# Performance work log

Measured on AMD Instinct MI355X. Metric: run time of the kernel, lower is better.

## Reference

```python
import jax, jax.numpy as jnp
import numpy as np

C = 256
EPS = 1e-5


def dwconv3x3(x, w):
    # x: [B,C,H,W], w: [C,1,3,3] depthwise (groups=C)
    return jax.lax.conv_general_dilated(
        x, w, window_strides=(1, 1), padding=((1, 1), (1, 1)),
        dimension_numbers=('NCHW', 'OIHW', 'NCHW'), feature_group_count=x.shape[1])


def bn(x, gamma, beta, mean, var):
    # inference-mode batchnorm over channel dim of NCHW
    inv = gamma * jax.lax.rsqrt(var + EPS)
    return x * inv[:, None, None] + (beta - mean * inv)[:, None, None]


def setup_inputs() -> dict:
    key = jax.random.key(0)
    ks = jax.random.split(key, 8)
    B, H, W = 32, 64, 64
    inp = {
        'x': jax.random.normal(ks[0], (B, C, H, W), jnp.float32),
        'edge_w': jax.random.normal(ks[1], (C, 1, 3, 3), jnp.float32) * 0.1,
        'edge_gamma': jnp.ones((C,), jnp.float32),
        'edge_beta': jnp.zeros((C,), jnp.float32),
        'edge_mean': jnp.zeros((C,), jnp.float32),
        'edge_var': jnp.ones((C,), jnp.float32),
        'fc1_w': jax.random.normal(ks[2], (C // 16, C), jnp.float32) * 0.05,
        'fc2_w': jax.random.normal(ks[3], (C, C // 16), jnp.float32) * 0.05,
        'fusion_w': jax.random.normal(ks[4], (C, 2 * C), jnp.float32) * 0.05,
        'fusion_b': jnp.zeros((C,), jnp.float32),
        'bn1_gamma': jnp.ones((C,), jnp.float32),
        'bn1_beta': jnp.zeros((C,), jnp.float32),
        'bn1_mean': jnp.zeros((C,), jnp.float32),
        'bn1_var': jnp.ones((C,), jnp.float32),
        'deform_w': jax.random.normal(ks[5], (C, 1, 3, 3), jnp.float32) * 0.1,
        'balance_w': jax.random.normal(ks[6], (C, C), jnp.float32) * 0.05,
        'balance_b': jnp.zeros((C,), jnp.float32),
        'bn2_gamma': jnp.ones((C,), jnp.float32),
        'bn2_beta': jnp.zeros((C,), jnp.float32),
        'bn2_mean': jnp.zeros((C,), jnp.float32),
        'bn2_var': jnp.ones((C,), jnp.float32),
    }
    return inp


def reference(x, edge_w, edge_gamma, edge_beta, edge_mean, edge_var,
              fc1_w, fc2_w, fusion_w, fusion_b,
              bn1_gamma, bn1_beta, bn1_mean, bn1_var,
              deform_w, balance_w, balance_b,
              bn2_gamma, bn2_beta, bn2_mean, bn2_var):
    # --- EdgeEnhancementAttention ---
    edge = jax.nn.relu(bn(dwconv3x3(x, edge_w), edge_gamma, edge_beta, edge_mean, edge_var))
    # SE channel attention
    avg = jnp.mean(x, axis=(2, 3))                       # [B,C]
    att = jax.nn.relu(avg @ fc1_w.T)                     # [B,C/16]
    att = jax.nn.sigmoid(att @ fc2_w.T)                  # [B,C]
    enhanced = x * att[:, :, None, None]
    fused = jnp.concatenate([enhanced, edge], axis=1)    # [B,2C,H,W]
    out = jnp.einsum('bchw,oc->bohw', fused, fusion_w) + fusion_b[None, :, None, None]
    out = bn(out, bn1_gamma, bn1_beta, bn1_mean, bn1_var)
    # --- DeformConv2d with zero offsets == plain depthwise 3x3 conv, no bias ---
    out = dwconv3x3(out, deform_w)
    # --- balance: 1x1 conv + BN, then gate by input ---
    out = jnp.einsum('bchw,oc->bohw', out, balance_w) + balance_b[None, :, None, None]
    out = bn(out, bn2_gamma, bn2_beta, bn2_mean, bn2_var)
    return out * x
```

## Files before the change

kernel.cpp:

```cpp
#include <hip/hip_runtime.h>
#include <math.h>

#define HW 4096
#define PLSTRIDE ((size_t)HW * 8)

typedef unsigned short ushort_t;
typedef short v8s __attribute__((ext_vector_type(8)));
typedef float v4f __attribute__((ext_vector_type(4)));

__device__ __forceinline__ float bf2f(ushort_t u) {
    union { unsigned int i; float f; } v; v.i = ((unsigned int)u) << 16; return v.f;
}
__device__ __forceinline__ ushort_t f2bf(float f) {
    unsigned int x = __float_as_uint(f);
    x += 0x7fffu + ((x >> 16) & 1u);
    return (ushort_t)(x >> 16);
}

__device__ __forceinline__ void gld16(const ushort_t* g, ushort_t* l) {
    __builtin_amdgcn_global_load_lds(
        (__attribute__((address_space(1))) void*)g,
        (__attribute__((address_space(3))) void*)l, 16, 0, 0);
}

__global__ __launch_bounds__(256) void k_consts(
    const float* eg, const float* ebt, const float* em, const float* ev,
    const float* fb,
    const float* g1, const float* b1, const float* m1, const float* v1,
    const float* balb,
    const float* g2, const float* b2, const float* m2, const float* v2,
    float* cbuf)
{
    int c = threadIdx.x;
    float iE = eg[c] * rsqrtf(ev[c] + 1e-5f);
    cbuf[c]       = iE;
    cbuf[256 + c] = ebt[c] - em[c] * iE;
    float i1 = g1[c] * rsqrtf(v1[c] + 1e-5f);
    cbuf[512 + c] = i1;
    cbuf[768 + c] = b1[c] - m1[c] * i1 + fb[c] * i1;
    float i2 = g2[c] * rsqrtf(v2[c] + 1e-5f);
    cbuf[1024 + c] = i2;
    cbuf[1280 + c] = b2[c] - m2[c] * i2 + balb[c] * i2;
}

__global__ __launch_bounds__(256) void k_wcopy(const float* fusw, const float* balw,
                                               ushort_t* fusw2b, ushort_t* balwb)
{
    int o = blockIdx.x, t = threadIdx.x;
    fusw2b[o * 256 + t] = f2bf(fusw[o * 512 + 256 + t]);
    balwb[o * 256 + t]  = f2bf(balw[o * 256 + t]);
}

__global__ __launch_bounds__(512) void k_edge(const float* x, const float* ew,
                                              const float* cbuf, ushort_t* A,
                                              float* avg)
{
    __shared__ __align__(16) ushort_t Xs[4096];
    __shared__ __align__(16) ushort_t Es[4096];
    int cg = blockIdx.x;
    int b = blockIdx.y;
    int t = threadIdx.x;
    int w = t & 63;
    int pl = t >> 6;
    int c = cg * 8 + pl;
    const float* px = x + ((size_t)(b * 256 + c)) * HW;
    ushort_t* AX = A + ((size_t)(b * 64 + cg)) * PLSTRIDE;
    ushort_t* AE = A + ((size_t)(b * 64 + 32 + cg)) * PLSTRIDE;
    float wt[9];
    #pragma unroll
    for (int k = 0; k < 9; ++k) wt[k] = ew[c * 9 + k];
    float sE = cbuf[c], cE = cbuf[256 + c];
    bool wl = (w > 0), wrr = (w < 63);

    float p0l = 0.f, p0c = 0.f, p0r = 0.f;
    float p1l, p1c, p1r;
    p1c = px[w];
    p1l = wl ? px[w - 1] : 0.f;
    p1r = wrr ? px[w + 1] : 0.f;
    float s = 0.f;
    for (int hb = 0; hb < 8; ++hb) {
        #pragma unroll
        for (int hi = 0; hi < 8; ++hi) {
            int h = hb * 8 + hi;
            float p2l, p2c, p2r;
            if (h < 63) {
                const float* row = px + (h + 1) * 64;
                p2c = row[w];
                p2l = wl ? row[w - 1] : 0.f;
                p2r = wrr ? row[w + 1] : 0.f;
            } else {
                p2l = p2c = p2r = 0.f;
            }
            float a = p0l * wt[0] + p0c * wt[1] + p0r * wt[2]
                    + p1l * wt[3] + p1c * wt[4] + p1r * wt[5]
                    + p2l * wt[6] + p2c * wt[7] + p2r * wt[8];
            s += p1c;
            float v = a * sE + cE;
            Es[hi * 512 + w * 8 + pl] = f2bf(v > 0.f ? v : 0.f);
            Xs[hi * 512 + w * 8 + pl] = f2bf(p1c);
            p0l = p1l; p0c = p1c; p0r = p1r;
            p1l = p2l; p1c = p2c; p1r = p2r;
        }
        __syncthreads();
        {
            int hwg = (hb * 8 + pl) * 64 + w;
            uint4 vx = *(const uint4*)&Xs[pl * 512 + w * 8];
            uint4 ve = *(const uint4*)&Es[pl * 512 + w * 8];
            *(uint4*)(AX + (size_t)hwg * 8) = vx;
            *(uint4*)(AE + (size_t)hwg * 8) = ve;
        }
        __syncthreads();
    }
    #pragma unroll
    for (int off = 32; off > 0; off >>= 1) s += __shfl_down(s, off, 64);
    if ((t & 63) == 0) avg[b * 256 + c] = s * (1.0f / HW);
}

__global__ __launch_bounds__(256) void k_sefold(const float* avg, const float* fc1,
                                                const float* fc2, const float* fusw,
                                                ushort_t* w1b)
{
    int b = blockIdx.x, t = threadIdx.x;
    __shared__ float av[256];
    __shared__ float hid[16];
    av[t] = avg[b * 256 + t];
    __syncthreads();
    if (t < 16) {
        float h = 0.f;
        for (int c = 0; c < 256; ++c) h += av[c] * fc1[t * 256 + c];
        hid[t] = h > 0.f ? h : 0.f;
    }
    __syncthreads();
    float a = 0.f;
    #pragma unroll
    for (int j = 0; j < 16; ++j) a += hid[j] * fc2[t * 16 + j];
    float att = 1.0f / (1.0f + expf(-a));
    ushort_t* wout = w1b + (size_t)b * 65536;
    for (int o = 0; o < 256; ++o)
        wout[o * 256 + t] = f2bf(fusw[o * 512 + t] * att);
}

__global__ __launch_bounds__(512) void k_gemm1(ushort_t* A, const ushort_t* w1b,
                                               const ushort_t* fusw2b,
                                               const float* cbuf)
{
    __shared__ __align__(16) ushort_t At[2][128 * 64];
    int hw0 = blockIdx.x * 128;
    int b = blockIdx.y;
    int t = threadIdx.x;
    int lane = t & 63, wv = t >> 6;
    int quad = lane >> 4, l16 = lane & 15;
    int wr = wv >> 2, wc = wv & 3;

    v4f acc[4][4];
    #pragma unroll
    for (int i = 0; i < 4; ++i)
        #pragma unroll
        for (int j = 0; j < 4; ++j) acc[i][j] = (v4f){0.f, 0.f, 0.f, 0.f};

    const ushort_t* rowA[4];
    const ushort_t* rowB[4];
    int oo[4];
    #pragma unroll
    for (int nt = 0; nt < 4; ++nt) {
        int o = wc * 64 + nt * 16 + l16;
        oo[nt] = o;
        rowA[nt] = w1b + ((size_t)(b * 256 + o)) * 256;
        rowB[nt] = fusw2b + (size_t)o * 256;
    }

    int mrow0 = wv * 16 + (lane >> 3);
    int cswz = (lane & 7) ^ (mrow0 & 7);
    const ushort_t* srcK = A + ((size_t)(b * 64 + cswz)) * PLSTRIDE
                             + ((size_t)(hw0 + mrow0)) * 8;

#define STAGE1(bs, kbv) { \
    const ushort_t* sp = srcK + (size_t)((kbv) * 8) * PLSTRIDE; \
    gld16(sp, &At[bs][(wv * 16) * 64]); \
    gld16(sp + 64, &At[bs][(wv * 16 + 8) * 64]); }

#define LDB1(dst, kbv) { \
    _Pragma("unroll") for (int ks2 = 0; ks2 < 2; ++ks2) { \
        int kg = (kbv) * 64 + ks2 * 32 + quad * 8; \
        _Pragma("unroll") for (int nt = 0; nt < 4; ++nt) { \
            dst[ks2][nt] = ((kbv) < 4) ? *(const v8s*)(rowA[nt] + kg) \
                                       : *(const v8s*)(rowB[nt] + (kg - 256)); \
        } } }

#define COMP1(bs, bsrc) { \
    _Pragma("unroll") for (int ks2 = 0; ks2 < 2; ++ks2) { \
        v8s afr[4]; \
        _Pragma("unroll") for (int mt = 0; mt < 4; ++mt) { \
            int ml = wr * 64 + mt * 16 + l16; \
            int jj = (ks2 * 4 + quad) ^ (ml & 7); \
            afr[mt] = *(const v8s*)(&At[bs][ml * 64 + jj * 8]); \
        } \
        _Pragma("unroll") for (int mt = 0; mt < 4; ++mt) \
            _Pragma("unroll") for (int nt = 0; nt < 4; ++nt) \
                acc[mt][nt] = __builtin_amdgcn_mfma_f32_16x16x32_bf16( \
                    afr[mt], bsrc[ks2][nt], acc[mt][nt], 0, 0, 0); \
    } }

    v8s bq0[2][4], bq1[2][4];
    LDB1(bq0, 0);
    STAGE1(0, 0);
    __syncthreads();
    #pragma unroll
    for (int kb = 0; kb < 8; ++kb) {
        if ((kb & 1) == 0) {
            if (kb < 7) { STAGE1(1, kb + 1); LDB1(bq1, kb + 1); }
            COMP1(0, bq0);
        } else {
            if (kb < 7) { STAGE1(0, kb + 1); LDB1(bq0, kb + 1); }
            COMP1(1, bq1);
        }
        __syncthreads();
    }
#undef STAGE1
#undef LDB1
#undef COMP1

    #pragma unroll
    for (int nt = 0; nt < 4; ++nt) {
        int o = oo[nt];
        float s1 = cbuf[512 + o], c1 = cbuf[768 + o];
        ushort_t* op = A + ((size_t)(b * 64 + 32 + (o >> 3))) * PLSTRIDE + (o & 7);
        #pragma unroll
        for (int mt = 0; mt < 4; ++mt)
            #pragma unroll
            for (int r = 0; r < 4; ++r) {
                int m = hw0 + wr * 64 + mt * 16 + quad * 4 + r;
                op[(size_t)m * 8] = f2bf(acc[mt][nt][r] * s1 + c1);
            }
    }
}

__global__ __launch_bounds__(256) void k_dw2(ushort_t* A, const float* dfw)
{
    int h = blockIdx.x;
    int b = blockIdx.y;
    int t = threadIdx.x;
    int wc = t & 7;
    int cg = t >> 3;
    int c0 = cg * 8;
    int w0 = wc * 8;

    float acc[8][8];
    #pragma unroll
    for (int w = 0; w < 8; ++w)
        #pragma unroll
        for (int ch = 0; ch < 8; ++ch) acc[w][ch] = 0.f;

    const ushort_t* pE = A + ((size_t)(b * 64 + 32 + cg)) * PLSTRIDE;
    #pragma unroll
    for (int r = 0; r < 3; ++r) {
        int hh = h - 1 + r;
        if (hh < 0 || hh > 63) continue;
        float wtr[3][8];
        #pragma unroll
        for (int d = 0; d < 3; ++d)
            #pragma unroll
            for (int ch = 0; ch < 8; ++ch)
                wtr[d][ch] = dfw[(c0 + ch) * 9 + r * 3 + d];
        const ushort_t* row = pE + (size_t)(hh * 64) * 8;
        uint4 rv[10];
        #pragma unroll
        for (int j = 0; j < 10; ++j) {
            int col = w0 - 1 + j;
            if (col >= 0 && col < 64)
                rv[j] = *(const uint4*)(row + (size_t)col * 8);
            else
                rv[j] = (uint4){0u, 0u, 0u, 0u};
        }
        #pragma unroll
        for (int j = 0; j < 10; ++j) {
            unsigned int wd[4] = { rv[j].x, rv[j].y, rv[j].z, rv[j].w };
            float v[8];
            #pragma unroll
            for (int i = 0; i < 8; ++i)
                v[i] = bf2f((i & 1) ? (ushort_t)(wd[i >> 1] >> 16)
                                    : (ushort_t)(wd[i >> 1] & 0xffff));
            if (j <= 7)
                #pragma unroll
                for (int ch = 0; ch < 8; ++ch) acc[j][ch] += v[ch] * wtr[0][ch];
            if (j >= 1 && j <= 8)
                #pragma unroll
                for (int ch = 0; ch < 8; ++ch) acc[j - 1][ch] += v[ch] * wtr[1][ch];
            if (j >= 2)
                #pragma unroll
                for (int ch = 0; ch < 8; ++ch) acc[j - 2][ch] += v[ch] * wtr[2][ch];
        }
    }
    ushort_t* pX = A + ((size_t)(b * 64 + cg)) * PLSTRIDE + (size_t)(h * 64 + w0) * 8;
    #pragma unroll
    for (int w = 0; w < 8; ++w) {
        uint4 ov;
        ov.x = (unsigned int)f2bf(acc[w][0]) | ((unsigned int)f2bf(acc[w][1]) << 16);
        ov.y = (unsigned int)f2bf(acc[w][2]) | ((unsigned int)f2bf(acc[w][3]) << 16);
        ov.z = (unsigned int)f2bf(acc[w][4]) | ((unsigned int)f2bf(acc[w][5]) << 16);
        ov.w = (unsigned int)f2bf(acc[w][6]) | ((unsigned int)f2bf(acc[w][7]) << 16);
        *(uint4*)(pX + (size_t)w * 8) = ov;
    }
}

__global__ __launch_bounds__(512) void k_gemm2(ushort_t* A, const ushort_t* balwb)
{
    __shared__ __align__(16) ushort_t At[2][128 * 64];
    int hw0 = blockIdx.x * 128;
    int b = blockIdx.y;
    int t = threadIdx.x;
    int lane = t & 63, wv = t >> 6;
    int quad = lane >> 4, l16 = lane & 15;
    int wr = wv >> 2, wc = wv & 3;

    v4f acc[4][4];
    #pragma unroll
    for (int i = 0; i < 4; ++i)
        #pragma unroll
        for (int j = 0; j < 4; ++j) acc[i][j] = (v4f){0.f, 0.f, 0.f, 0.f};

    const ushort_t* rowW[4];
    int oo[4];
    #pragma unroll
    for (int nt = 0; nt < 4; ++nt) {
        int o = wc * 64 + nt * 16 + l16;
        oo[nt] = o;
        rowW[nt] = balwb + (size_t)o * 256;
    }

    int mrow0 = wv * 16 + (lane >> 3);
    int cswz = (lane & 7) ^ (mrow0 & 7);
    const ushort_t* srcK = A + ((size_t)(b * 64 + cswz)) * PLSTRIDE
                             + ((size_t)(hw0 + mrow0)) * 8;

#define STAGE2(bs, kbv) { \
    const ushort_t* sp = srcK + (size_t)((kbv) * 8) * PLSTRIDE; \
    gld16(sp, &At[bs][(wv * 16) * 64]); \
    gld16(sp + 64, &At[bs][(wv * 16 + 8) * 64]); }

#define LDB2(dst, kbv) { \
    _Pragma("unroll") for (int ks2 = 0; ks2 < 2; ++ks2) { \
        int kg = (kbv) * 64 + ks2 * 32 + quad * 8; \
        _Pragma("unroll") for (int nt = 0; nt < 4; ++nt) \
            dst[ks2][nt] = *(const v8s*)(rowW[nt] + kg); \
    } }

#define COMP2(bs, bsrc) { \
    _Pragma("unroll") for (int ks2 = 0; ks2 < 2; ++ks2) { \
        v8s afr[4]; \
        _Pragma("unroll") for (int mt = 0; mt < 4; ++mt) { \
            int ml = wr * 64 + mt * 16 + l16; \
            int jj = (ks2 * 4 + quad) ^ (ml & 7); \
            afr[mt] = *(const v8s*)(&At[bs][ml * 64 + jj * 8]); \
        } \
        _Pragma("unroll") for (int mt = 0; mt < 4; ++mt) \
            _Pragma("unroll") for (int nt = 0; nt < 4; ++nt) \
                acc[mt][nt] = __builtin_amdgcn_mfma_f32_16x16x32_bf16( \
                    afr[mt], bsrc[ks2][nt], acc[mt][nt], 0, 0, 0); \
    } }

    v8s bq0[2][4], bq1[2][4];
    LDB2(bq0, 0);
    STAGE2(0, 0);
    __syncthreads();
    #pragma unroll
    for (int kb = 0; kb < 4; ++kb) {
        if ((kb & 1) == 0) {
            if (kb < 3) { STAGE2(1, kb + 1); LDB2(bq1, kb + 1); }
            COMP2(0, bq0);
        } else {
            if (kb < 3) { STAGE2(0, kb + 1); LDB2(bq0, kb + 1); }
            COMP2(1, bq1);
        }
        __syncthreads();
    }
#undef STAGE2
#undef LDB2
#undef COMP2

    #pragma unroll
    for (int nt = 0; nt < 4; ++nt) {
        int o = oo[nt];
        ushort_t* op = A + ((size_t)(b * 64 + 32 + (o >> 3))) * PLSTRIDE + (o & 7);
        #pragma unroll
        for (int mt = 0; mt < 4; ++mt)
            #pragma unroll
            for (int r = 0; r < 4; ++r) {
                int m = hw0 + wr * 64 + mt * 16 + quad * 4 + r;
                op[(size_t)m * 8] = f2bf(acc[mt][nt][r]);
            }
    }
}

__global__ __launch_bounds__(256) void k_final(const ushort_t* A, const float* x,
                                               const float* cbuf, float* out)
{
    __shared__ float Lt[64 * 65];
    int bid = blockIdx.x;
    int b = bid >> 8;
    int rem = bid & 255;
    int hw0 = (rem >> 2) * 64;
    int c0 = (rem & 3) * 64;
    int t = threadIdx.x;
    #pragma unroll
    for (int r = 0; r < 2; ++r) {
        int idx = r * 256 + t;
        int hwl = idx >> 3;
        int cq = idx & 7;
        uint4 v = *(const uint4*)(A + ((size_t)(b * 64 + 32 + (c0 >> 3) + cq)) * PLSTRIDE
                                    + (size_t)(hw0 + hwl) * 8);
        unsigned int wd[4] = { v.x, v.y, v.z, v.w };
        #pragma unroll
        for (int j = 0; j < 8; ++j) {
            ushort_t u = (j & 1) ? (ushort_t)(wd[j >> 1] >> 16) : (ushort_t)(wd[j >> 1] & 0xffff);
            Lt[(cq * 8 + j) * 65 + hwl] = bf2f(u);
        }
    }
    __syncthreads();
    int hw_l = t & 63;
    int c_l0 = t >> 6;
    #pragma unroll
    for (int j = 0; j < 16; ++j) {
        int c_l = c_l0 * 16 + j;
        int c = c0 + c_l;
        float s2 = cbuf[1024 + c], c2 = cbuf[1280 + c];
        size_t g = ((size_t)b * 256 + c) * HW + hw0 + hw_l;
        float xv = x[g];
        out[g] = (Lt[c_l * 65 + hw_l] * s2 + c2) * xv;
    }
}

extern "C" void kernel_launch(void* const* d_in, const int* in_sizes, int n_in,
                              void* d_out, int out_size, void* d_ws, size_t ws_size,
                              hipStream_t stream)
{
    const float* x    = (const float*)d_in[0];
    const float* ew   = (const float*)d_in[1];
    const float* fc1  = (const float*)d_in[6];
    const float* fc2  = (const float*)d_in[7];
    const float* fusw = (const float*)d_in[8];
    const float* dfw  = (const float*)d_in[14];
    const float* balw = (const float*)d_in[15];
    float* out = (float*)d_out;

    char* ws = (char*)d_ws;
    ushort_t* A      = (ushort_t*)(ws);
    ushort_t* w1b    = (ushort_t*)(ws + 134217728);
    ushort_t* fusw2b = (ushort_t*)(ws + 138412032);
    ushort_t* balwb  = (ushort_t*)(ws + 138543104);
    float*    avg    = (float*)(ws + 138674176);
    float*    cbuf   = (float*)(ws + 138706944);

    k_consts<<<1, 256, 0, stream>>>((const float*)d_in[2], (const float*)d_in[3],
                                    (const float*)d_in[4], (const float*)d_in[5],
                                    (const float*)d_in[9],
                                    (const float*)d_in[10], (const float*)d_in[11],
                                    (const float*)d_in[12], (const float*)d_in[13],
                                    (const float*)d_in[16],
                                    (const float*)d_in[17], (const float*)d_in[18],
                                    (const float*)d_in[19], (const float*)d_in[20],
                                    cbuf);
    k_wcopy<<<256, 256, 0, stream>>>(fusw, balw, fusw2b, balwb);
    k_edge<<<dim3(32, 32), 512, 0, stream>>>(x, ew, cbuf, A, avg);
    k_sefold<<<32, 256, 0, stream>>>(avg, fc1, fc2, fusw, w1b);
    k_gemm1<<<dim3(32, 32), 512, 0, stream>>>(A, w1b, fusw2b, cbuf);
    k_dw2<<<dim3(64, 32), 256, 0, stream>>>(A, dfw);
    k_gemm2<<<dim3(32, 32), 512, 0, stream>>>(A, balwb);
    k_final<<<8192, 256, 0, stream>>>(A, x, cbuf, out);
}
```

Baseline: 609.2 us.

## Preload whole K-slab into LDS up front in both 1x1 GEMM kernels

Both GEMM kernels now issue all global-to-LDS loads for the full K range at the start, which removes the double-buffered staging and the per-iteration barriers. Only one barrier remains before the compute loop, which is now not unrolled. gemm1 halves its M tile to 64 rows so the eight 64x64 LDS buffers fit, and the grid doubles to compensate. The cost is more LDS per block (64KB), which may lower occupancy, and for gemm1 the smaller tile means less reuse of the weight loads.

```diff
diff --git a/kernel.cpp b/kernel.cpp
--- a/kernel.cpp
+++ b/kernel.cpp
@@ -140,21 +140,30 @@
         wout[o * 256 + t] = f2bf(fusw[o * 512 + t] * att);
 }
 
-__global__ __launch_bounds__(512) void k_gemm1(ushort_t* A, const ushort_t* w1b,
-                                               const ushort_t* fusw2b,
-                                               const float* cbuf)
-{
-    __shared__ __align__(16) ushort_t At[2][128 * 64];
-    int hw0 = blockIdx.x * 128;
+__global__ __launch_bounds__(512) void k_gemm1(ushort_t* __restrict__ A,
+                                               const ushort_t* __restrict__ w1b,
+                                               const ushort_t* __restrict__ fusw2b,
+                                               const float* __restrict__ cbuf)
+{
+    __shared__ __align__(16) ushort_t At[8][64 * 64];
+    int hw0 = blockIdx.x * 64;
     int b = blockIdx.y;
     int t = threadIdx.x;
     int lane = t & 63, wv = t >> 6;
     int quad = lane >> 4, l16 = lane & 15;
     int wr = wv >> 2, wc = wv & 3;
 
-    v4f acc[4][4];
-    #pragma unroll
-    for (int i = 0; i < 4; ++i)
+    int mrow0 = wv * 8 + (lane >> 3);
+    int cswz = (lane & 7) ^ (mrow0 & 7);
+    const ushort_t* srcK = A + ((size_t)(b * 64 + cswz)) * PLSTRIDE
+                             + ((size_t)(hw0 + mrow0)) * 8;
+    #pragma unroll
+    for (int kb = 0; kb < 8; ++kb)
+        gld16(srcK + (size_t)(kb * 8) * PLSTRIDE, &At[kb][wv * 8 * 64]);
+
+    v4f acc[2][4];
+    #pragma unroll
+    for (int i = 0; i < 2; ++i)
         #pragma unroll
         for (int j = 0; j < 4; ++j) acc[i][j] = (v4f){0.f, 0.f, 0.f, 0.f};
 
@@ -168,16 +177,6 @@
         rowA[nt] = w1b + ((size_t)(b * 256 + o)) * 256;
         rowB[nt] = fusw2b + (size_t)o * 256;
     }
-
-    int mrow0 = wv * 16 + (lane >> 3);
-    int cswz = (lane & 7) ^ (mrow0 & 7);
-    const ushort_t* srcK = A + ((size_t)(b * 64 + cswz)) * PLSTRIDE
-                             + ((size_t)(hw0 + mrow0)) * 8;
-
-#define STAGE1(bs, kbv) { \
-    const ushort_t* sp = srcK + (size_t)((kbv) * 8) * PLSTRIDE; \
-    gld16(sp, &At[bs][(wv * 16) * 64]); \
-    gld16(sp + 64, &At[bs][(wv * 16 + 8) * 64]); }
 
 #define LDB1(dst, kbv) { \
     _Pragma("unroll") for (int ks2 = 0; ks2 < 2; ++ks2) { \
@@ -187,15 +186,15 @@
                                        : *(const v8s*)(rowB[nt] + (kg - 256)); \
         } } }
 
-#define COMP1(bs, bsrc) { \
+#define COMP1(kbv, bsrc) { \
     _Pragma("unroll") for (int ks2 = 0; ks2 < 2; ++ks2) { \
-        v8s afr[4]; \
-        _Pragma("unroll") for (int mt = 0; mt < 4; ++mt) { \
-            int ml = wr * 64 + mt * 16 + l16; \
+        v8s afr[2]; \
+        _Pragma("unroll") for (int mt = 0; mt < 2; ++mt) { \
+            int ml = wr * 32 + mt * 16 + l16; \
             int jj = (ks2 * 4 + quad) ^ (ml & 7); \
-            afr[mt] = *(const v8s*)(&At[bs][ml * 64 + jj * 8]); \
+            afr[mt] = *(const v8s*)(&At[kbv][ml * 64 + jj * 8]); \
         } \
-        _Pragma("unroll") for (int mt = 0; mt < 4; ++mt) \
+        _Pragma("unroll") for (int mt = 0; mt < 2; ++mt) \
             _Pragma("unroll") for (int nt = 0; nt < 4; ++nt) \
                 acc[mt][nt] = __builtin_amdgcn_mfma_f32_16x16x32_bf16( \
                     afr[mt], bsrc[ks2][nt], acc[mt][nt], 0, 0, 0); \
@@ -203,20 +202,14 @@
 
     v8s bq0[2][4], bq1[2][4];
     LDB1(bq0, 0);
-    STAGE1(0, 0);
     __syncthreads();
-    #pragma unroll
-    for (int kb = 0; kb < 8; ++kb) {
-        if ((kb & 1) == 0) {
-            if (kb < 7) { STAGE1(1, kb + 1); LDB1(bq1, kb + 1); }
-            COMP1(0, bq0);
-        } else {
-            if (kb < 7) { STAGE1(0, kb + 1); LDB1(bq0, kb + 1); }
-            COMP1(1, bq1);
-        }
-        __syncthreads();
-    }
-#undef STAGE1
+    #pragma unroll 1
+    for (int kb = 0; kb < 8; kb += 2) {
+        LDB1(bq1, kb + 1);
+        COMP1(kb, bq0);
+        if (kb < 6) LDB1(bq0, kb + 2);
+        COMP1(kb + 1, bq1);
+    }
 #undef LDB1
 #undef COMP1
 
@@ -226,10 +219,10 @@
         float s1 = cbuf[512 + o], c1 = cbuf[768 + o];
         ushort_t* op = A + ((size_t)(b * 64 + 32 + (o >> 3))) * PLSTRIDE + (o & 7);
         #pragma unroll
-        for (int mt = 0; mt < 4; ++mt)
+        for (int mt = 0; mt < 2; ++mt)
             #pragma unroll
             for (int r = 0; r < 4; ++r) {
-                int m = hw0 + wr * 64 + mt * 16 + quad * 4 + r;
+                int m = hw0 + wr * 32 + mt * 16 + quad * 4 + r;
                 op[(size_t)m * 8] = f2bf(acc[mt][nt][r] * s1 + c1);
             }
     }
@@ -303,9 +296,10 @@
     }
 }
 
-__global__ __launch_bounds__(512) void k_gemm2(ushort_t* A, const ushort_t* balwb)
-{
-    __shared__ __align__(16) ushort_t At[2][128 * 64];
+__global__ __launch_bounds__(512) void k_gemm2(ushort_t* __restrict__ A,
+                                               const ushort_t* __restrict__ balwb)
+{
+    __shared__ __align__(16) ushort_t At[4][128 * 64];
     int hw0 = blockIdx.x * 128;
     int b = blockIdx.y;
     int t = threadIdx.x;
@@ -313,6 +307,17 @@
     int quad = lane >> 4, l16 = lane & 15;
     int wr = wv >> 2, wc = wv & 3;
 
+    int mrow0 = wv * 16 + (lane >> 3);
+    int cswz = (lane & 7) ^ (mrow0 & 7);
+    const ushort_t* srcK = A + ((size_t)(b * 64 + cswz)) * PLSTRIDE
+                             + ((size_t)(hw0 + mrow0)) * 8;
+    #pragma unroll
+    for (int kb = 0; kb < 4; ++kb) {
+        const ushort_t* sp = srcK + (size_t)(kb * 8) * PLSTRIDE;
+        gld16(sp, &At[kb][(wv * 16) * 64]);
+        gld16(sp + 64, &At[kb][(wv * 16 + 8) * 64]);
+    }
+
     v4f acc[4][4];
     #pragma unroll
     for (int i = 0; i < 4; ++i)
@@ -327,16 +332,6 @@
         oo[nt] = o;
         rowW[nt] = balwb + (size_t)o * 256;
     }
-
-    int mrow0 = wv * 16 + (lane >> 3);
-    int cswz = (lane & 7) ^ (mrow0 & 7);
-    const ushort_t* srcK = A + ((size_t)(b * 64 + cswz)) * PLSTRIDE
-                             + ((size_t)(hw0 + mrow0)) * 8;
-
-#define STAGE2(bs, kbv) { \
-    const ushort_t* sp = srcK + (size_t)((kbv) * 8) * PLSTRIDE; \
-    gld16(sp, &At[bs][(wv * 16) * 64]); \
-    gld16(sp + 64, &At[bs][(wv * 16 + 8) * 64]); }
 
 #define LDB2(dst, kbv) { \
     _Pragma("unroll") for (int ks2 = 0; ks2 < 2; ++ks2) { \
@@ -345,13 +340,13 @@
             dst[ks2][nt] = *(const v8s*)(rowW[nt] + kg); \
     } }
 
-#define COMP2(bs, bsrc) { \
+#define COMP2(kbv, bsrc) { \
     _Pragma("unroll") for (int ks2 = 0; ks2 < 2; ++ks2) { \
         v8s afr[4]; \
         _Pragma("unroll") for (int mt = 0; mt < 4; ++mt) { \
             int ml = wr * 64 + mt * 16 + l16; \
             int jj = (ks2 * 4 + quad) ^ (ml & 7); \
-            afr[mt] = *(const v8s*)(&At[bs][ml * 64 + jj * 8]); \
+            afr[mt] = *(const v8s*)(&At[kbv][ml * 64 + jj * 8]); \
         } \
         _Pragma("unroll") for (int mt = 0; mt < 4; ++mt) \
             _Pragma("unroll") for (int nt = 0; nt < 4; ++nt) \
@@ -361,20 +356,14 @@
 
     v8s bq0[2][4], bq1[2][4];
     LDB2(bq0, 0);
-    STAGE2(0, 0);
     __syncthreads();
-    #pragma unroll
-    for (int kb = 0; kb < 4; ++kb) {
-        if ((kb & 1) == 0) {
-            if (kb < 3) { STAGE2(1, kb + 1); LDB2(bq1, kb + 1); }
-            COMP2(0, bq0);
-        } else {
-            if (kb < 3) { STAGE2(0, kb + 1); LDB2(bq0, kb + 1); }
-            COMP2(1, bq1);
-        }
-        __syncthreads();
-    }
-#undef STAGE2
+    #pragma unroll 1
+    for (int kb = 0; kb < 4; kb += 2) {
+        LDB2(bq1, kb + 1);
+        COMP2(kb, bq0);
+        if (kb < 2) LDB2(bq0, kb + 2);
+        COMP2(kb + 1, bq1);
+    }
 #undef LDB2
 #undef COMP2
 
@@ -463,7 +452,7 @@
     k_wcopy<<<256, 256, 0, stream>>>(fusw, balw, fusw2b, balwb);
     k_edge<<<dim3(32, 32), 512, 0, stream>>>(x, ew, cbuf, A, avg);
     k_sefold<<<32, 256, 0, stream>>>(avg, fc1, fc2, fusw, w1b);
-    k_gemm1<<<dim3(32, 32), 512, 0, stream>>>(A, w1b, fusw2b, cbuf);
+    k_gemm1<<<dim3(64, 32), 512, 0, stream>>>(A, w1b, fusw2b, cbuf);
     k_dw2<<<dim3(64, 32), 256, 0, stream>>>(A, dfw);
     k_gemm2<<<dim3(32, 32), 512, 0, stream>>>(A, balwb);
     k_final<<<8192, 256, 0, stream>>>(A, x, cbuf, out);
```

Measured after the change: 648.5 us. 6.5% more time.
